# Kernel optimization log

Hardware: AMD Instinct MI355X
Metric: run time of the kernel (lower is better)

## Reference

```python
import jax, jax.numpy as jnp
import numpy as np

B, T, D, H = 2, 2048, 1024, 16
HD = D // H
FF = 4 * D
EPS = 1e-5


def rmsnorm(x, w):
    var = jnp.mean(jnp.square(x), axis=-1, keepdims=True)
    return x * jax.lax.rsqrt(var + EPS) * w


def setup_inputs() -> dict:
    key = jax.random.key(0)
    ks = jax.random.split(key, 17)
    sc = 0.02
    d = {}
    d["x"] = jax.random.normal(ks[0], (B, T, D), jnp.float32)
    d["x_token"] = jax.random.normal(ks[1], (B, T, D), jnp.float32)
    d["pos_emb"] = jax.random.normal(ks[2], (T, D), jnp.float32)
    d["lc_weight"] = jax.random.normal(ks[3], (1,), jnp.float32)
    d["Wq"] = jax.random.normal(ks[4], (D, D), jnp.float32) * sc  # per-head query weights stacked
    d["Wk"] = jax.random.normal(ks[5], (D, D), jnp.float32) * sc
    d["Wv"] = jax.random.normal(ks[6], (D, D), jnp.float32) * sc
    d["proj_w"] = jax.random.normal(ks[7], (D, D), jnp.float32) * sc
    d["proj_b"] = jnp.zeros((D,), jnp.float32)
    d["w1_w"] = jax.random.normal(ks[8], (FF, D), jnp.float32) * sc
    d["w1_b"] = jnp.zeros((FF,), jnp.float32)
    d["w2_w"] = jax.random.normal(ks[9], (D, FF), jnp.float32) * sc
    d["w2_b"] = jnp.zeros((D,), jnp.float32)
    d["w3_w"] = jax.random.normal(ks[10], (FF, D), jnp.float32) * sc
    d["w3_b"] = jnp.zeros((FF,), jnp.float32)
    d["norm1_w"] = jnp.ones((D,), jnp.float32)
    d["norm2_w"] = jnp.ones((D,), jnp.float32)
    return d


def reference(x, x_token, pos_emb, lc_weight, Wq, Wk, Wv, proj_w, proj_b,
              w1_w, w1_b, w2_w, w2_b, w3_w, w3_b, norm1_w, norm2_w):
    lc = jax.nn.sigmoid(lc_weight)  # scalar gate
    x_att = lc * x + (1.0 - lc) * x_token
    xn = rmsnorm(x_att, norm1_w)

    # q, v from normed gated input; k from raw positional embedding (faithful to source)
    q = (xn @ Wq.T).reshape(B, T, H, HD)
    k = (pos_emb @ Wk.T).reshape(T, H, HD)
    v = (xn @ Wv.T).reshape(B, T, H, HD)

    # NOTE: scale uses full model dim E (=D), not head_size, as in the source
    scores = jnp.einsum('bqhd,khd->bhqk', q, k) * (D ** -0.5)
    causal = jnp.tril(jnp.ones((T, T), bool))
    scores = jnp.where(causal, scores, -jnp.inf)
    p = jax.nn.softmax(scores, axis=-1)
    attn = jnp.einsum('bhqk,bkhd->bqhd', p, v).reshape(B, T, D)

    x = x + attn @ proj_w.T + proj_b

    xn2 = rmsnorm(x, norm2_w)
    h = jax.nn.silu(xn2 @ w1_w.T + w1_b) * (xn2 @ w3_w.T + w3_b)
    return x + h @ w2_w.T + w2_b
```

## Files before the change

kernel.cpp:

```cpp
#include <hip/hip_runtime.h>
#include <hip/hip_bf16.h>


typedef __hip_bfloat16 bf16;
typedef __attribute__((ext_vector_type(8))) short bf16x8;
typedef __attribute__((ext_vector_type(4))) float floatx4;

constexpr int cB = 2, cT = 2048, cD = 1024, cH = 16, cFF = 4096;
constexpr float cEPS = 1e-5f;
constexpr unsigned BF16_ONES = 0x3F803F80u;

__device__ __forceinline__ float b2f(bf16 x) { return __bfloat162float(x); }
__device__ __forceinline__ bf16  f2b(float x) { return __float2bfloat16(x); }
__device__ __forceinline__ unsigned short f2bu(float x) {
  bf16 t = __float2bfloat16(x);
  union { bf16 b; unsigned short u; } cv;
  cv.b = t;
  return cv.u;
}
__device__ __forceinline__ float loadR(const bf16* p)  { return b2f(*p); }
__device__ __forceinline__ float loadR(const float* p) { return *p; }

__device__ __forceinline__ void gload16(const bf16* g, unsigned short* l) {
  __builtin_amdgcn_global_load_lds(
      (const __attribute__((address_space(1))) void*)g,
      (__attribute__((address_space(3))) void*)l, 16, 0, 0);
}

__device__ __forceinline__ void xcd_remap(int& bx, int& by, int gx, int gy) {
  const int nwg = gx * gy;
  const int lin = by * gx + bx;
  const int nl  = (lin & 7) * (nwg >> 3) + (lin >> 3);
  bx = nl % gx;
  by = nl / gx;
}

struct ConvArgs {
  const void* src[17];
  bf16* dst[17];
  int n[17];
  int sb[17];
};

__global__ __launch_bounds__(256) void convert_all_k(ConvArgs a) {
  const int bid = blockIdx.x;
  int seg = 0;
#pragma unroll
  for (int i = 1; i < 17; i++) seg = (bid >= a.sb[i]) ? i : seg;
  const int n = a.n[seg];
  const int i0 = (bid - a.sb[seg]) * 2048 + threadIdx.x * 8;
  if (i0 >= n) return;
  const bool isb = (((const unsigned*)a.src[15])[0] == BF16_ONES);
  const void* src = a.src[seg];
  bf16* dst = a.dst[seg];
  if (i0 + 8 <= n) {
    if (isb) {
      *(int4*)(dst + i0) = *(const int4*)((const bf16*)src + i0);
    } else {
      float4 f0 = *(const float4*)((const float*)src + i0);
      float4 f1 = *(const float4*)((const float*)src + i0 + 4);
      int4 ro;
      bf16* po = (bf16*)&ro;
      po[0] = f2b(f0.x); po[1] = f2b(f0.y); po[2] = f2b(f0.z); po[3] = f2b(f0.w);
      po[4] = f2b(f1.x); po[5] = f2b(f1.y); po[6] = f2b(f1.z); po[7] = f2b(f1.w);
      *(int4*)(dst + i0) = ro;
    }
  } else {
    for (int j = i0; j < n; j++)
      dst[j] = isb ? ((const bf16*)src)[j] : f2b(((const float*)src)[j]);
  }
}

template <int TN, int OUTK, typename ResT>
__device__ __forceinline__ void gemm_core(
    const bf16* __restrict__ A, const bf16* __restrict__ W,
    const bf16* __restrict__ bias, const ResT* __restrict__ R,
    void* __restrict__ Cv, const unsigned* __restrict__ dbits,
    int crow0, int N, int K, int m0, int n0,
    unsigned short* As, unsigned short* Bs)
{
  constexpr int NTN = TN / 32;
  const int tid  = threadIdx.x;
  const int wave = tid >> 6;
  const int lane = tid & 63;
  const int l15  = lane & 15;
  const int quad = lane >> 4;
  const int wm   = (wave >> 1) * 64;
  const int wn   = (wave & 1) * (TN / 2);

  bool obf = (OUTK != 1);
  if (OUTK == 2) obf = (*dbits == BF16_ONES);

  const int lr  = lane >> 2;
  const int lc8 = (lane & 3) * 8;
  const bf16* Ag0 = A + (size_t)(m0 + wave * 32 + lr) * K + lc8;
  const bf16* Ag1 = Ag0 + (size_t)16 * K;
  unsigned short* lA0 = &As[(wave * 32) * 32];
  unsigned short* lA1 = &As[(wave * 32 + 16) * 32];
  const bf16* Bg0 = W + (size_t)(n0 + wave * (TN / 4) + lr) * K + lc8;
  const bf16* Bg1 = Bg0 + (size_t)16 * K;
  unsigned short* lB0 = &Bs[(wave * (TN / 4)) * 32];
  unsigned short* lB1 = &Bs[(wave * (TN / 4) + 16) * 32];

  floatx4 acc[4][NTN];
#pragma unroll
  for (int i = 0; i < 4; i++)
#pragma unroll
    for (int j = 0; j < NTN; j++) acc[i][j] = (floatx4){0.f, 0.f, 0.f, 0.f};

  for (int k0 = 0; k0 < K; k0 += 32) {
    gload16(Ag0 + k0, lA0);
    gload16(Ag1 + k0, lA1);
    gload16(Bg0 + k0, lB0);
    if (TN == 128) gload16(Bg1 + k0, lB1);
    __syncthreads();

    bf16x8 a[4], b[NTN];
#pragma unroll
    for (int t = 0; t < 4; t++)
      a[t] = *(const bf16x8*)&As[(wm + t * 16 + l15) * 32 + quad * 8];
#pragma unroll
    for (int t = 0; t < NTN; t++)
      b[t] = *(const bf16x8*)&Bs[(wn + t * 16 + l15) * 32 + quad * 8];
#pragma unroll
    for (int tm = 0; tm < 4; tm++)
#pragma unroll
      for (int tn = 0; tn < NTN; tn++)
        acc[tm][tn] = __builtin_amdgcn_mfma_f32_16x16x32_bf16(a[tm], b[tn], acc[tm][tn], 0, 0, 0);
    __syncthreads();
  }

#pragma unroll
  for (int tm = 0; tm < 4; tm++) {
#pragma unroll
    for (int tn = 0; tn < NTN; tn++) {
      const int row = m0 + wm + tm * 16 + quad * 4;
      const int col = n0 + wn + tn * 16 + l15;
      float bv = bias ? b2f(bias[col]) : 0.f;
#pragma unroll
      for (int i = 0; i < 4; i++) {
        float val = acc[tm][tn][i] + bv;
        const size_t ridx = (size_t)(row + i) * N + col;
        const size_t cidx = (size_t)(crow0 + row + i) * N + col;
        if (R) val += loadR(&R[ridx]);
        if (OUTK == 0)      ((bf16*)Cv)[cidx] = f2b(val);
        else if (OUTK == 1) ((float*)Cv)[cidx] = val;
        else { if (obf) ((bf16*)Cv)[cidx] = f2b(val); else ((float*)Cv)[cidx] = val; }
      }
    }
  }
}

template <int TN, int OUTK, typename ResT>
__global__ __launch_bounds__(256) void gemm_t(
    const bf16* __restrict__ A, const bf16* __restrict__ W,
    const bf16* __restrict__ bias, const ResT* __restrict__ R,
    void* __restrict__ Cv, const unsigned* __restrict__ dbits,
    int crow0, int M, int N, int K)
{
  __shared__ __align__(16) unsigned short As[128 * 32];
  __shared__ __align__(16) unsigned short Bs[TN * 32];
  int bx = blockIdx.x, by = blockIdx.y;
  xcd_remap(bx, by, gridDim.x, gridDim.y);
  gemm_core<TN, OUTK, ResT>(A, W, bias, R, Cv, dbits, crow0, N, K,
                            by * 128, bx * TN, As, Bs);
}

__global__ __launch_bounds__(256) void gemm_qkv(
    const bf16* __restrict__ xn, const bf16* __restrict__ pos,
    const bf16* __restrict__ Wq, const bf16* __restrict__ Wv,
    const bf16* __restrict__ Wk,
    bf16* __restrict__ q, bf16* __restrict__ v, bf16* __restrict__ kb)
{
  const int z = blockIdx.z;
  int bx = blockIdx.x, by = blockIdx.y;
  xcd_remap(bx, by, gridDim.x, gridDim.y);
  if (z == 2 && by >= 16) return;
  __shared__ __align__(16) unsigned short As[128 * 32];
  __shared__ __align__(16) unsigned short Bs[128 * 32];
  const bf16* A = (z == 2) ? pos : xn;
  const bf16* W = (z == 0) ? Wq : (z == 1) ? Wv : Wk;
  bf16* C = (z == 0) ? q : (z == 1) ? v : kb;
  gemm_core<128, 0, bf16>(A, W, nullptr, (const bf16*)nullptr, C, nullptr, 0,
                          cD, cD, by * 128, bx * 128, As, Bs);
}

__global__ __launch_bounds__(256, 2) void gemm_w13(
    const bf16* __restrict__ A,
    const bf16* __restrict__ W1, const bf16* __restrict__ b1,
    const bf16* __restrict__ W3, const bf16* __restrict__ b3,
    bf16* __restrict__ H, int N, int K)
{
  __shared__ __align__(16) unsigned short As[128 * 32];
  __shared__ __align__(16) unsigned short B1s[128 * 32];
  __shared__ __align__(16) unsigned short B3s[128 * 32];
  const int tid  = threadIdx.x;
  int bx = blockIdx.x, by = blockIdx.y;
  xcd_remap(bx, by, gridDim.x, gridDim.y);
  const int m0   = by * 128;
  const int n0   = bx * 128;
  const int wave = tid >> 6;
  const int lane = tid & 63;
  const int l15  = lane & 15;
  const int quad = lane >> 4;
  const int wm   = (wave >> 1) * 64;
  const int wn   = (wave & 1) * 64;

  const int lr  = lane >> 2;
  const int lc8 = (lane & 3) * 8;
  const bf16* Ag0  = A  + (size_t)(m0 + wave * 32 + lr) * K + lc8;
  const bf16* Ag1  = Ag0 + (size_t)16 * K;
  const bf16* B1g0 = W1 + (size_t)(n0 + wave * 32 + lr) * K + lc8;
  const bf16* B1g1 = B1g0 + (size_t)16 * K;
  const bf16* B3g0 = W3 + (size_t)(n0 + wave * 32 + lr) * K + lc8;
  const bf16* B3g1 = B3g0 + (size_t)16 * K;
  unsigned short* lA0 = &As[(wave * 32) * 32];
  unsigned short* lA1 = &As[(wave * 32 + 16) * 32];
  unsigned short* l10 = &B1s[(wave * 32) * 32];
  unsigned short* l11 = &B1s[(wave * 32 + 16) * 32];
  unsigned short* l30 = &B3s[(wave * 32) * 32];
  unsigned short* l31 = &B3s[(wave * 32 + 16) * 32];

  floatx4 acc1[4][4], acc3[4][4];
#pragma unroll
  for (int i = 0; i < 4; i++)
#pragma unroll
    for (int j = 0; j < 4; j++) {
      acc1[i][j] = (floatx4){0.f, 0.f, 0.f, 0.f};
      acc3[i][j] = (floatx4){0.f, 0.f, 0.f, 0.f};
    }

  for (int k0 = 0; k0 < K; k0 += 32) {
    gload16(Ag0 + k0, lA0);
    gload16(Ag1 + k0, lA1);
    gload16(B1g0 + k0, l10);
    gload16(B1g1 + k0, l11);
    gload16(B3g0 + k0, l30);
    gload16(B3g1 + k0, l31);
    __syncthreads();

    bf16x8 a[4], v1[4], v3[4];
#pragma unroll
    for (int t = 0; t < 4; t++) {
      a[t]  = *(const bf16x8*)&As[(wm + t * 16 + l15) * 32 + quad * 8];
      v1[t] = *(const bf16x8*)&B1s[(wn + t * 16 + l15) * 32 + quad * 8];
      v3[t] = *(const bf16x8*)&B3s[(wn + t * 16 + l15) * 32 + quad * 8];
    }
#pragma unroll
    for (int tm = 0; tm < 4; tm++)
#pragma unroll
      for (int tn = 0; tn < 4; tn++) {
        acc1[tm][tn] = __builtin_amdgcn_mfma_f32_16x16x32_bf16(a[tm], v1[tn], acc1[tm][tn], 0, 0, 0);
        acc3[tm][tn] = __builtin_amdgcn_mfma_f32_16x16x32_bf16(a[tm], v3[tn], acc3[tm][tn], 0, 0, 0);
      }
    __syncthreads();
  }

#pragma unroll
  for (int tm = 0; tm < 4; tm++) {
#pragma unroll
    for (int tn = 0; tn < 4; tn++) {
      const int row = m0 + wm + tm * 16 + quad * 4;
      const int col = n0 + wn + tn * 16 + l15;
      const float bv1 = b2f(b1[col]);
      const float bv3 = b2f(b3[col]);
#pragma unroll
      for (int i = 0; i < 4; i++) {
        float g = acc1[tm][tn][i] + bv1;
        float u = acc3[tm][tn][i] + bv3;
        float val = g * (1.f / (1.f + __expf(-g))) * u;
        H[(size_t)(row + i) * N + col] = f2b(val);
      }
    }
  }
}

template <bool GATE, typename InT>
__global__ __launch_bounds__(256) void rmsnorm_k(
    const InT* __restrict__ X, const bf16* __restrict__ XT,
    const bf16* __restrict__ LC, const bf16* __restrict__ Wn,
    bf16* __restrict__ O)
{
  const int row = blockIdx.x;
  const int tid = threadIdx.x;
  const size_t base = (size_t)row * cD;
  const int c = tid * 4;

  float lc = 1.f, lc1 = 0.f;
  if (GATE) {
    float g = b2f(LC[0]);
    lc = 1.f / (1.f + __expf(-g));
    lc1 = 1.f - lc;
  }

  float xv[4];
  if (sizeof(InT) == 2) {
    ushort4 u = *(const ushort4*)((const unsigned short*)X + base + c);
    const bf16* pu = (const bf16*)&u;
#pragma unroll
    for (int i = 0; i < 4; i++) xv[i] = b2f(pu[i]);
  } else {
    float4 f = *(const float4*)((const float*)X + base + c);
    xv[0] = f.x; xv[1] = f.y; xv[2] = f.z; xv[3] = f.w;
  }
  if (GATE) {
    ushort4 u = *(const ushort4*)((const unsigned short*)XT + base + c);
    const bf16* pu = (const bf16*)&u;
#pragma unroll
    for (int i = 0; i < 4; i++) xv[i] = lc * xv[i] + lc1 * b2f(pu[i]);
  }

  float ss = xv[0] * xv[0] + xv[1] * xv[1] + xv[2] * xv[2] + xv[3] * xv[3];
#pragma unroll
  for (int off = 32; off; off >>= 1) ss += __shfl_xor(ss, off, 64);

  __shared__ float red[4];
  if ((tid & 63) == 0) red[tid >> 6] = ss;
  __syncthreads();
  float tot = red[0] + red[1] + red[2] + red[3];
  float rs = rsqrtf(tot * (1.f / cD) + cEPS);

  ushort4 o;
  bf16* po = (bf16*)&o;
#pragma unroll
  for (int i = 0; i < 4; i++) po[i] = f2b(xv[i] * rs * b2f(Wn[c + i]));
  *(ushort4*)((unsigned short*)O + base + c) = o;
}

__global__ __launch_bounds__(256) void fattn_k(
    const bf16* __restrict__ Q, const bf16* __restrict__ K,
    const bf16* __restrict__ V, bf16* __restrict__ O)
{
  constexpr int LQ = 72, LK = 72, LV = 72;
  __shared__ __align__(16) unsigned short Qs[64 * LQ];
  __shared__ __align__(16) unsigned short Ks[64 * LK];
  __shared__ __align__(16) unsigned short Vs[64 * LV];

  const int tid  = threadIdx.x;
  const int wave = tid >> 6;
  const int lane = tid & 63;
  const int l15  = lane & 15;
  const int quad = lane >> 4;
  const int blk  = blockIdx.x;
  const int qt   = 31 - (blk & 31);
  const int h    = (blk >> 5) & 15;
  const int b    = blk >> 9;
  const int q0   = qt * 64;

  const bf16* Qb = Q + ((size_t)b * cT) * cD + h * 64;
  const bf16* Kb = K + h * 64;
  const bf16* Vb = V + ((size_t)b * cT) * cD + h * 64;

  {
    const int qr = tid >> 2, qc = (tid & 3) * 16;
    const bf16* gq = Qb + (size_t)(q0 + qr) * cD + qc;
    *(int4*)&Qs[qr * LQ + qc]     = *(const int4*)(gq);
    *(int4*)&Qs[qr * LQ + qc + 8] = *(const int4*)(gq + 8);
  }
  __syncthreads();

  const int qw = wave * 16;
  bf16x8 qa[2];
#pragma unroll
  for (int dc = 0; dc < 2; dc++)
    qa[dc] = *(const bf16x8*)&Qs[(qw + l15) * LQ + dc * 32 + quad * 8];

  float l_p[4] = {0.f, 0.f, 0.f, 0.f};
  floatx4 oacc[4];
#pragma unroll
  for (int dt = 0; dt < 4; dt++) oacc[dt] = (floatx4){0.f, 0.f, 0.f, 0.f};

  const int ktiles = qt + 1;
  unsigned short* Pw = &Qs[qw * LQ];

  const int kr = tid >> 2, kc = (tid & 3) * 16;
  int4 kpre0, kpre1;
  unsigned short vpre[16];
  {
    const bf16* g = Kb + (size_t)kr * cD + kc;
    kpre0 = *(const int4*)g;
    kpre1 = *(const int4*)(g + 8);
    const unsigned short* gv = (const unsigned short*)(Vb + (size_t)(wave * 16) * cD + lane);
#pragma unroll
    for (int j = 0; j < 16; j++) vpre[j] = gv[(size_t)j * cD];
  }

  for (int it = 0; it < ktiles; ++it) {
    const int k0 = it * 64;
    __syncthreads();
    *(int4*)&Ks[kr * LK + kc]     = kpre0;
    *(int4*)&Ks[kr * LK + kc + 8] = kpre1;
    {
      union { unsigned short us[8]; int4 v4; } pk0, pk1;
#pragma unroll
      for (int j = 0; j < 8; j++) { pk0.us[j] = vpre[j]; pk1.us[j] = vpre[8 + j]; }
      *(int4*)&Vs[lane * LV + wave * 16]     = pk0.v4;
      *(int4*)&Vs[lane * LV + wave * 16 + 8] = pk1.v4;
    }
    __syncthreads();

    if (it + 1 < ktiles) {
      const bf16* g = Kb + (size_t)(k0 + 64 + kr) * cD + kc;
      kpre0 = *(const int4*)g;
      kpre1 = *(const int4*)(g + 8);
      const unsigned short* gv = (const unsigned short*)(Vb + (size_t)(k0 + 64 + wave * 16) * cD + lane);
#pragma unroll
      for (int j = 0; j < 16; j++) vpre[j] = gv[(size_t)j * cD];
    }

    floatx4 s[4];
#pragma unroll
    for (int st = 0; st < 4; st++) {
      bf16x8 kb0 = *(const bf16x8*)&Ks[(st * 16 + l15) * LK + quad * 8];
      bf16x8 kb1 = *(const bf16x8*)&Ks[(st * 16 + l15) * LK + 32 + quad * 8];
      s[st] = (floatx4){0.f, 0.f, 0.f, 0.f};
      s[st] = __builtin_amdgcn_mfma_f32_16x16x32_bf16(qa[0], kb0, s[st], 0, 0, 0);
      s[st] = __builtin_amdgcn_mfma_f32_16x16x32_bf16(qa[1], kb1, s[st], 0, 0, 0);
    }
    float p[4][4];
#pragma unroll
    for (int i = 0; i < 4; i++) {
      const int qrow = q0 + qw + quad * 4 + i;
#pragma unroll
      for (int st = 0; st < 4; st++) {
        const int kp = k0 + st * 16 + l15;
        float pv = (kp > qrow) ? 0.f : __expf(s[st][i] * 0.03125f);
        p[st][i] = pv;
        l_p[i] += pv;
      }
    }
#pragma unroll
    for (int st = 0; st < 4; st++)
#pragma unroll
      for (int i = 0; i < 4; i++)
        Pw[(quad * 4 + i) * LQ + st * 16 + l15] = f2bu(p[st][i]);
    bf16x8 pa[2];
#pragma unroll
    for (int pc = 0; pc < 2; pc++)
      pa[pc] = *(const bf16x8*)&Pw[l15 * LQ + pc * 32 + quad * 8];
#pragma unroll
    for (int dt = 0; dt < 4; dt++) {
      bf16x8 vb0 = *(const bf16x8*)&Vs[(dt * 16 + l15) * LV + quad * 8];
      bf16x8 vb1 = *(const bf16x8*)&Vs[(dt * 16 + l15) * LV + 32 + quad * 8];
      oacc[dt] = __builtin_amdgcn_mfma_f32_16x16x32_bf16(pa[0], vb0, oacc[dt], 0, 0, 0);
      oacc[dt] = __builtin_amdgcn_mfma_f32_16x16x32_bf16(pa[1], vb1, oacc[dt], 0, 0, 0);
    }
  }

  float rl[4];
#pragma unroll
  for (int i = 0; i < 4; i++) {
    float li = l_p[i];
#pragma unroll
    for (int off = 1; off < 16; off <<= 1) li += __shfl_xor(li, off, 64);
    rl[i] = 1.f / li;
  }
  const size_t obase = ((size_t)b * cT + q0 + qw) * cD + h * 64;
#pragma unroll
  for (int dt = 0; dt < 4; dt++)
#pragma unroll
    for (int i = 0; i < 4; i++)
      O[obase + (size_t)(quad * 4 + i) * cD + dt * 16 + l15] = f2b(oacc[dt][i] * rl[i]);
}

extern "C" void kernel_launch(void* const* d_in, const int* in_sizes, int n_in,
                              void* d_out, int out_size, void* d_ws, size_t ws_size,
                              hipStream_t stream) {
  char* ws = (char*)d_ws;
  const size_t MB = 1u << 20;
  const int BT = cB * cT;

  bf16* cxt  = (bf16*)(ws + 0);
  bf16* cpos = (bf16*)(ws + 8 * MB);
  bf16* q    = (bf16*)(ws + 12 * MB);
  bf16* kbuf = (bf16*)(ws + 20 * MB);
  bf16* v    = (bf16*)(ws + 24 * MB);
  bf16* h    = (bf16*)(ws + 0);
  size_t off = 32 * MB;
  auto alloc = [&](size_t bytes) -> char* {
    char* p = ws + off;
    off = (off + bytes + 255) & ~(size_t)255;
    return p;
  };
  bf16*  cx  = (bf16*)alloc((size_t)BT * cD * 2);
  bf16*  xn  = (bf16*)alloc((size_t)BT * cD * 2);
  float* x2  = (float*)alloc((size_t)BT * cD * 4);
  bf16*  xn2 = (bf16*)alloc((size_t)BT * cD * 2);
  bf16* cin[17];
  cin[0] = cx; cin[1] = cxt; cin[2] = cpos;
  for (int i = 3; i < 17; i++) cin[i] = (bf16*)alloc((size_t)in_sizes[i] * 2);

  const unsigned* dbits = (const unsigned*)d_in[15];
  dim3 blk(256);

  ConvArgs ca;
  int nblk = 0;
  for (int i = 0; i < 17; i++) {
    ca.src[i] = d_in[i];
    ca.dst[i] = cin[i];
    ca.n[i] = in_sizes[i];
    ca.sb[i] = nblk;
    nblk += (in_sizes[i] + 2047) / 2048;
  }
  convert_all_k<<<nblk, blk, 0, stream>>>(ca);

  const bf16 *clc = cin[3], *cWq = cin[4], *cWk = cin[5], *cWv = cin[6];
  const bf16 *cprojw = cin[7], *cprojb = cin[8];
  const bf16 *cw1w = cin[9], *cw1b = cin[10], *cw2w = cin[11], *cw2b = cin[12];
  const bf16 *cw3w = cin[13], *cw3b = cin[14], *cn1 = cin[15], *cn2 = cin[16];

  rmsnorm_k<true, bf16><<<BT, blk, 0, stream>>>(cx, cxt, clc, cn1, xn);
  gemm_qkv<<<dim3(cD / 128, BT / 128, 3), blk, 0, stream>>>(
      xn, cpos, cWq, cWv, cWk, q, v, kbuf);
  bf16* attn = xn;
  fattn_k<<<cB * cH * (cT / 64), blk, 0, stream>>>(q, kbuf, v, attn);
  gemm_t<128, 1, bf16><<<dim3(cD / 128, BT / 128), blk, 0, stream>>>(
      attn, cprojw, cprojb, cx, x2, nullptr, 0, BT, cD, cD);
  rmsnorm_k<false, float><<<BT, blk, 0, stream>>>(
      x2, (const bf16*)nullptr, (const bf16*)nullptr, cn2, xn2);
  gemm_w13<<<dim3(cFF / 128, BT / 128), blk, 0, stream>>>(
      xn2, cw1w, cw1b, cw3w, cw3b, h, cFF, cD);
  gemm_t<128, 2, float><<<dim3(cD / 128, BT / 128), blk, 0, stream>>>(
      h, cw2w, cw2b, x2, d_out, dbits, 0, BT, cD, cFF);
  (void)n_in; (void)out_size; (void)ws_size;
}
```

Measured before the change: 510.0 us.

## Use 128x64 tiles with K=64 steps and split-K atomics for W2 GEMM

Replaces the 128x128 GEMM core with a 128x64 tile that loads two 32-wide K slices per iteration, halving the number of barriers per K. The QKV and projection GEMMs get more blocks (better CU fill on a small grid), and the W2 GEMM is split into two K-chunks that accumulate into a zeroed fp32 buffer via atomics, followed by a combine kernel adding residual and bias. It trades extra atomic traffic, a zeroing pass in rmsnorm, and an extra launch for higher occupancy; K-tile reuse of A drops with the narrower N tile.

```diff
diff --git a/kernel.cpp b/kernel.cpp
--- a/kernel.cpp
+++ b/kernel.cpp
@@ -27,10 +27,13 @@
       (__attribute__((address_space(3))) void*)l, 16, 0, 0);
 }
 
+__device__ __forceinline__ int xcd_remap1(int lin, int n) {
+  return (lin & 7) * (n >> 3) + (lin >> 3);
+}
 __device__ __forceinline__ void xcd_remap(int& bx, int& by, int gx, int gy) {
   const int nwg = gx * gy;
   const int lin = by * gx + bx;
-  const int nl  = (lin & 7) * (nwg >> 3) + (lin >> 3);
+  const int nl  = xcd_remap1(lin, nwg);
   bx = nl % gx;
   by = nl / gx;
 }
@@ -71,99 +74,103 @@
   }
 }
 
-template <int TN, int OUTK, typename ResT>
-__device__ __forceinline__ void gemm_core(
+template <int OUTK, typename ResT>
+__device__ __forceinline__ void gemm_core64(
     const bf16* __restrict__ A, const bf16* __restrict__ W,
     const bf16* __restrict__ bias, const ResT* __restrict__ R,
-    void* __restrict__ Cv, const unsigned* __restrict__ dbits,
-    int crow0, int N, int K, int m0, int n0,
+    void* __restrict__ Cv,
+    int N, int Kst, int kb, int klen, int m0, int n0,
     unsigned short* As, unsigned short* Bs)
 {
-  constexpr int NTN = TN / 32;
   const int tid  = threadIdx.x;
   const int wave = tid >> 6;
   const int lane = tid & 63;
   const int l15  = lane & 15;
   const int quad = lane >> 4;
   const int wm   = (wave >> 1) * 64;
-  const int wn   = (wave & 1) * (TN / 2);
-
-  bool obf = (OUTK != 1);
-  if (OUTK == 2) obf = (*dbits == BF16_ONES);
+  const int wn   = (wave & 1) * 32;
 
   const int lr  = lane >> 2;
   const int lc8 = (lane & 3) * 8;
-  const bf16* Ag0 = A + (size_t)(m0 + wave * 32 + lr) * K + lc8;
-  const bf16* Ag1 = Ag0 + (size_t)16 * K;
+  const bf16* Ag0 = A + (size_t)(m0 + wave * 32 + lr) * Kst + kb + lc8;
+  const bf16* Ag1 = Ag0 + (size_t)16 * Kst;
+  const bf16* Bg0 = W + (size_t)(n0 + wave * 16 + lr) * Kst + kb + lc8;
   unsigned short* lA0 = &As[(wave * 32) * 32];
   unsigned short* lA1 = &As[(wave * 32 + 16) * 32];
-  const bf16* Bg0 = W + (size_t)(n0 + wave * (TN / 4) + lr) * K + lc8;
-  const bf16* Bg1 = Bg0 + (size_t)16 * K;
-  unsigned short* lB0 = &Bs[(wave * (TN / 4)) * 32];
-  unsigned short* lB1 = &Bs[(wave * (TN / 4) + 16) * 32];
-
-  floatx4 acc[4][NTN];
+  unsigned short* lB0 = &Bs[(wave * 16) * 32];
+
+  floatx4 acc[4][2];
 #pragma unroll
   for (int i = 0; i < 4; i++)
 #pragma unroll
-    for (int j = 0; j < NTN; j++) acc[i][j] = (floatx4){0.f, 0.f, 0.f, 0.f};
-
-  for (int k0 = 0; k0 < K; k0 += 32) {
+    for (int j = 0; j < 2; j++) acc[i][j] = (floatx4){0.f, 0.f, 0.f, 0.f};
+
+  for (int k0 = 0; k0 < klen; k0 += 64) {
     gload16(Ag0 + k0, lA0);
     gload16(Ag1 + k0, lA1);
+    gload16(Ag0 + k0 + 32, lA0 + 128 * 32);
+    gload16(Ag1 + k0 + 32, lA1 + 128 * 32);
     gload16(Bg0 + k0, lB0);
-    if (TN == 128) gload16(Bg1 + k0, lB1);
+    gload16(Bg0 + k0 + 32, lB0 + 64 * 32);
     __syncthreads();
 
-    bf16x8 a[4], b[NTN];
+    bf16x8 a[4][2], b[2][2];
 #pragma unroll
     for (int t = 0; t < 4; t++)
-      a[t] = *(const bf16x8*)&As[(wm + t * 16 + l15) * 32 + quad * 8];
-#pragma unroll
-    for (int t = 0; t < NTN; t++)
-      b[t] = *(const bf16x8*)&Bs[(wn + t * 16 + l15) * 32 + quad * 8];
+#pragma unroll
+      for (int kh = 0; kh < 2; kh++)
+        a[t][kh] = *(const bf16x8*)&As[kh * 128 * 32 + (wm + t * 16 + l15) * 32 + quad * 8];
+#pragma unroll
+    for (int u = 0; u < 2; u++)
+#pragma unroll
+      for (int kh = 0; kh < 2; kh++)
+        b[u][kh] = *(const bf16x8*)&Bs[kh * 64 * 32 + (wn + u * 16 + l15) * 32 + quad * 8];
 #pragma unroll
     for (int tm = 0; tm < 4; tm++)
 #pragma unroll
-      for (int tn = 0; tn < NTN; tn++)
-        acc[tm][tn] = __builtin_amdgcn_mfma_f32_16x16x32_bf16(a[tm], b[tn], acc[tm][tn], 0, 0, 0);
+      for (int tn = 0; tn < 2; tn++)
+#pragma unroll
+        for (int kh = 0; kh < 2; kh++)
+          acc[tm][tn] = __builtin_amdgcn_mfma_f32_16x16x32_bf16(a[tm][kh], b[tn][kh], acc[tm][tn], 0, 0, 0);
     __syncthreads();
   }
 
 #pragma unroll
   for (int tm = 0; tm < 4; tm++) {
 #pragma unroll
-    for (int tn = 0; tn < NTN; tn++) {
+    for (int tn = 0; tn < 2; tn++) {
       const int row = m0 + wm + tm * 16 + quad * 4;
       const int col = n0 + wn + tn * 16 + l15;
-      float bv = bias ? b2f(bias[col]) : 0.f;
+      float bv = (OUTK != 3 && bias) ? b2f(bias[col]) : 0.f;
 #pragma unroll
       for (int i = 0; i < 4; i++) {
         float val = acc[tm][tn][i] + bv;
-        const size_t ridx = (size_t)(row + i) * N + col;
-        const size_t cidx = (size_t)(crow0 + row + i) * N + col;
-        if (R) val += loadR(&R[ridx]);
-        if (OUTK == 0)      ((bf16*)Cv)[cidx] = f2b(val);
-        else if (OUTK == 1) ((float*)Cv)[cidx] = val;
-        else { if (obf) ((bf16*)Cv)[cidx] = f2b(val); else ((float*)Cv)[cidx] = val; }
+        const size_t cidx = (size_t)(row + i) * N + col;
+        if (OUTK == 3) {
+          atomicAdd((float*)Cv + cidx, val);
+        } else {
+          if (R) val += loadR(&R[cidx]);
+          if (OUTK == 0) ((bf16*)Cv)[cidx] = f2b(val);
+          else           ((float*)Cv)[cidx] = val;
+        }
       }
     }
   }
 }
 
-template <int TN, int OUTK, typename ResT>
-__global__ __launch_bounds__(256) void gemm_t(
+template <int OUTK, typename ResT>
+__global__ __launch_bounds__(256) void gemm_f(
     const bf16* __restrict__ A, const bf16* __restrict__ W,
     const bf16* __restrict__ bias, const ResT* __restrict__ R,
-    void* __restrict__ Cv, const unsigned* __restrict__ dbits,
-    int crow0, int M, int N, int K)
-{
-  __shared__ __align__(16) unsigned short As[128 * 32];
-  __shared__ __align__(16) unsigned short Bs[TN * 32];
-  int bx = blockIdx.x, by = blockIdx.y;
-  xcd_remap(bx, by, gridDim.x, gridDim.y);
-  gemm_core<TN, OUTK, ResT>(A, W, bias, R, Cv, dbits, crow0, N, K,
-                            by * 128, bx * TN, As, Bs);
+    void* __restrict__ Cv, int N, int Kst, int kchunk, int gx, int gxy)
+{
+  __shared__ __align__(16) unsigned short As[2 * 128 * 32];
+  __shared__ __align__(16) unsigned short Bs[2 * 64 * 32];
+  const int lin = xcd_remap1(blockIdx.x, gridDim.x);
+  const int kz  = lin / gxy;
+  const int rem = lin % gxy;
+  gemm_core64<OUTK, ResT>(A, W, bias, R, Cv, N, Kst, kz * kchunk, kchunk,
+                          (rem / gx) * 128, (rem % gx) * 64, As, Bs);
 }
 
 __global__ __launch_bounds__(256) void gemm_qkv(
@@ -172,17 +179,20 @@
     const bf16* __restrict__ Wk,
     bf16* __restrict__ q, bf16* __restrict__ v, bf16* __restrict__ kb)
 {
-  const int z = blockIdx.z;
-  int bx = blockIdx.x, by = blockIdx.y;
-  xcd_remap(bx, by, gridDim.x, gridDim.y);
-  if (z == 2 && by >= 16) return;
-  __shared__ __align__(16) unsigned short As[128 * 32];
-  __shared__ __align__(16) unsigned short Bs[128 * 32];
+  __shared__ __align__(16) unsigned short As[2 * 128 * 32];
+  __shared__ __align__(16) unsigned short Bs[2 * 64 * 32];
+  const int lin = xcd_remap1(blockIdx.x, gridDim.x);
+  int z, local;
+  if (lin < 512)       { z = 0; local = lin; }
+  else if (lin < 1024) { z = 1; local = lin - 512; }
+  else                 { z = 2; local = lin - 1024; }
+  const int gx = 16;
+  const int by = local / gx, bx = local % gx;
   const bf16* A = (z == 2) ? pos : xn;
   const bf16* W = (z == 0) ? Wq : (z == 1) ? Wv : Wk;
   bf16* C = (z == 0) ? q : (z == 1) ? v : kb;
-  gemm_core<128, 0, bf16>(A, W, nullptr, (const bf16*)nullptr, C, nullptr, 0,
-                          cD, cD, by * 128, bx * 128, As, Bs);
+  gemm_core64<0, bf16>(A, W, nullptr, (const bf16*)nullptr, C,
+                       cD, cD, 0, cD, by * 128, bx * 64, As, Bs);
 }
 
 __global__ __launch_bounds__(256, 2) void gemm_w13(
@@ -279,12 +289,14 @@
 __global__ __launch_bounds__(256) void rmsnorm_k(
     const InT* __restrict__ X, const bf16* __restrict__ XT,
     const bf16* __restrict__ LC, const bf16* __restrict__ Wn,
-    bf16* __restrict__ O)
+    bf16* __restrict__ O, float* __restrict__ Z)
 {
   const int row = blockIdx.x;
   const int tid = threadIdx.x;
   const size_t base = (size_t)row * cD;
   const int c = tid * 4;
+
+  if (Z) *(float4*)(Z + base + c) = (float4){0.f, 0.f, 0.f, 0.f};
 
   float lc = 1.f, lc1 = 0.f;
   if (GATE) {
@@ -325,6 +337,32 @@
 #pragma unroll
   for (int i = 0; i < 4; i++) po[i] = f2b(xv[i] * rs * b2f(Wn[c + i]));
   *(ushort4*)((unsigned short*)O + base + c) = o;
+}
+
+__global__ __launch_bounds__(256) void combine_k(
+    const float* __restrict__ P, const float* __restrict__ X2,
+    const bf16* __restrict__ bias, void* __restrict__ out,
+    const unsigned* __restrict__ dbits)
+{
+  const bool obf = (*dbits == BF16_ONES);
+  const size_t idx = ((size_t)blockIdx.x * 256 + threadIdx.x) * 4;
+  float4 p = *(const float4*)(P + idx);
+  float4 x = *(const float4*)(X2 + idx);
+  const int col = (int)(idx & (cD - 1));
+  ushort4 bu = *(const ushort4*)((const unsigned short*)bias + col);
+  const bf16* bb = (const bf16*)&bu;
+  float v0 = p.x + x.x + b2f(bb[0]);
+  float v1 = p.y + x.y + b2f(bb[1]);
+  float v2 = p.z + x.z + b2f(bb[2]);
+  float v3 = p.w + x.w + b2f(bb[3]);
+  if (obf) {
+    ushort4 o;
+    bf16* po = (bf16*)&o;
+    po[0] = f2b(v0); po[1] = f2b(v1); po[2] = f2b(v2); po[3] = f2b(v3);
+    *(ushort4*)((unsigned short*)out + idx) = o;
+  } else {
+    *(float4*)((float*)out + idx) = (float4){v0, v1, v2, v3};
+  }
 }
 
 __global__ __launch_bounds__(256) void fattn_k(
@@ -486,6 +524,7 @@
   bf16*  xn  = (bf16*)alloc((size_t)BT * cD * 2);
   float* x2  = (float*)alloc((size_t)BT * cD * 4);
   bf16*  xn2 = (bf16*)alloc((size_t)BT * cD * 2);
+  float* part = (float*)(ws + 32 * MB);
   bf16* cin[17];
   cin[0] = cx; cin[1] = cxt; cin[2] = cpos;
   for (int i = 3; i < 17; i++) cin[i] = (bf16*)alloc((size_t)in_sizes[i] * 2);
@@ -509,18 +548,18 @@
   const bf16 *cw1w = cin[9], *cw1b = cin[10], *cw2w = cin[11], *cw2b = cin[12];
   const bf16 *cw3w = cin[13], *cw3b = cin[14], *cn1 = cin[15], *cn2 = cin[16];
 
-  rmsnorm_k<true, bf16><<<BT, blk, 0, stream>>>(cx, cxt, clc, cn1, xn);
-  gemm_qkv<<<dim3(cD / 128, BT / 128, 3), blk, 0, stream>>>(
-      xn, cpos, cWq, cWv, cWk, q, v, kbuf);
+  rmsnorm_k<true, bf16><<<BT, blk, 0, stream>>>(cx, cxt, clc, cn1, xn, nullptr);
+  gemm_qkv<<<1280, blk, 0, stream>>>(xn, cpos, cWq, cWv, cWk, q, v, kbuf);
   bf16* attn = xn;
   fattn_k<<<cB * cH * (cT / 64), blk, 0, stream>>>(q, kbuf, v, attn);
-  gemm_t<128, 1, bf16><<<dim3(cD / 128, BT / 128), blk, 0, stream>>>(
-      attn, cprojw, cprojb, cx, x2, nullptr, 0, BT, cD, cD);
+  gemm_f<1, bf16><<<512, blk, 0, stream>>>(
+      attn, cprojw, cprojb, cx, x2, cD, cD, cD, 16, 512);
   rmsnorm_k<false, float><<<BT, blk, 0, stream>>>(
-      x2, (const bf16*)nullptr, (const bf16*)nullptr, cn2, xn2);
+      x2, (const bf16*)nullptr, (const bf16*)nullptr, cn2, xn2, part);
   gemm_w13<<<dim3(cFF / 128, BT / 128), blk, 0, stream>>>(
       xn2, cw1w, cw1b, cw3w, cw3b, h, cFF, cD);
-  gemm_t<128, 2, float><<<dim3(cD / 128, BT / 128), blk, 0, stream>>>(
-      h, cw2w, cw2b, x2, d_out, dbits, 0, BT, cD, cFF);
+  gemm_f<3, float><<<1024, blk, 0, stream>>>(
+      h, cw2w, nullptr, (const float*)nullptr, part, cD, cFF, 2048, 16, 512);
+  combine_k<<<BT, blk, 0, stream>>>(part, x2, cw2b, d_out, dbits);
   (void)n_in; (void)out_size; (void)ws_size;
 }
```

Result: faster. 466.9 us (-8.4%).
